# Performance work log

Measured on AMD Instinct MI355X. Metric: run time of the kernel, lower is better.

## Reference

```python
import jax, jax.numpy as jnp
import numpy as np

BN_EPS = 1e-5

def _conv(x, w, bias=None):
    # x: [N,C,H,W], w: [O,I,3,3], SAME padding, stride 1
    y = jax.lax.conv_general_dilated(x, w, window_strides=(1, 1),
                                     padding=((1, 1), (1, 1)),
                                     dimension_numbers=('NCHW', 'OIHW', 'NCHW'))
    if bias is not None:
        y = y + bias[None, :, None, None]
    return y

def _cconv(xr, xi, wr, wi):
    # complex conv: (xr + i xi) * (wr + i wi), cross-term combination
    return _conv(xr, wr) - _conv(xi, wi), _conv(xr, wi) + _conv(xi, wr)

def _bn1(x, g, b):
    # per-channel batchnorm (training-style stats over N,H,W)
    mu = jnp.mean(x, axis=(0, 2, 3), keepdims=True)
    var = jnp.var(x, axis=(0, 2, 3), keepdims=True)
    xh = (x - mu) * jax.lax.rsqrt(var + BN_EPS)
    return xh * g[None, :, None, None] + b[None, :, None, None]

def _cbn(xr, xi, g, b):
    # naive complex BN: normalize real/imag parts separately, shared affine
    return _bn1(xr, g, b), _bn1(xi, g, b)

def _crelu(xr, xi):
    return jax.nn.relu(xr), jax.nn.relu(xi)

def setup_inputs() -> dict:
    key = jax.random.key(0)
    ks = jax.random.split(key, 16)
    def w(k, o, i, kh=3, kw=3, s=0.05):
        return jax.random.normal(k, (o, i, kh, kw), jnp.float32) * s
    d = {}
    d['x'] = jax.random.normal(ks[0], (4, 256, 128, 224), jnp.float32)
    d['w1r'] = w(ks[1], 144, 256); d['w1i'] = w(ks[2], 144, 256)
    d['g1'] = jnp.ones((144,), jnp.float32); d['b1'] = jnp.zeros((144,), jnp.float32)
    d['w2r'] = w(ks[3], 96, 144); d['w2i'] = w(ks[4], 96, 144)
    d['g2'] = jnp.ones((96,), jnp.float32); d['b2'] = jnp.zeros((96,), jnp.float32)
    d['w3r'] = w(ks[5], 96, 96); d['w3i'] = w(ks[6], 96, 96)
    d['g3'] = jnp.ones((96,), jnp.float32); d['b3'] = jnp.zeros((96,), jnp.float32)
    d['w4r'] = w(ks[7], 96, 96); d['w4i'] = w(ks[8], 96, 96)
    d['g4'] = jnp.ones((96,), jnp.float32); d['b4'] = jnp.zeros((96,), jnp.float32)
    d['wc'] = w(ks[9], 1, 96); d['bc'] = jnp.zeros((1,), jnp.float32)
    d['wg'] = w(ks[10], 2, 96); d['bg'] = jnp.zeros((2,), jnp.float32)
    return d

def reference(x, w1r, w1i, g1, b1, w2r, w2i, g2, b2,
              w3r, w3i, g3, b3, w4r, w4i, g4, b4, wc, bc, wg, bg):
    # real input promoted to complex with zero imag
    xr, xi = x, jnp.zeros_like(x)
    xr, xi = _cconv(xr, xi, w1r, w1i)
    xr, xi = _cbn(xr, xi, g1, b1)
    xr, xi = _crelu(xr, xi)
    xr, xi = _cconv(xr, xi, w2r, w2i)
    xr, xi = _cbn(xr, xi, g2, b2)
    xr, xi = _crelu(xr, xi)
    xr, xi = _cconv(xr, xi, w3r, w3i)
    xr, xi = _cbn(xr, xi, g3, b3)
    xr, xi = _crelu(xr, xi)
    xr, xi = _cconv(xr, xi, w4r, w4i)
    xr, xi = _cbn(xr, xi, g4, b4)
    xr, xi = _crelu(xr, xi)
    x_mag = jnp.sqrt(xr * xr + xi * xi)  # torch.abs on complex
    cls = jax.nn.sigmoid(_conv(x_mag, wc, bc))
    reg = _conv(x_mag, wg, bg)
    return jnp.concatenate([cls, reg], axis=1)  # [N, 1+reg_layer, H, W]
```

## Files before the change

kernel.cpp:

```cpp
#include <hip/hip_runtime.h>
#include <cstdint>
#include <cstddef>

#define P_TOT 114688
#define W_IMG 224
#define H_IMG 128

typedef _Float16 f16;
typedef __attribute__((ext_vector_type(8))) _Float16 f16x8;
typedef __attribute__((ext_vector_type(4))) _Float16 f16x4;
typedef __attribute__((ext_vector_type(2))) _Float16 f16x2;
typedef __attribute__((ext_vector_type(4))) float f32x4;

#define WAITVM(N) asm volatile("s_waitcnt vmcnt(" #N ")" ::: "memory")

__device__ __forceinline__ void barrier_sync() {
  asm volatile("" ::: "memory");
  __builtin_amdgcn_s_barrier();
  asm volatile("" ::: "memory");
}

__device__ __forceinline__ void gload16(const void* g, void* l) {
  __builtin_amdgcn_global_load_lds((const __attribute__((address_space(1))) void*)g,
                                   (__attribute__((address_space(3))) void*)l, 16, 0, 0);
}

__global__ void k_pack_x(const float* __restrict__ x, f16* __restrict__ xb) {
  int tid = threadIdx.x;
  int pw  = tid & 15;
  int c8  = tid >> 4;
  int p   = blockIdx.x * 16 + pw;
  int w   = p % W_IMG;
  int h   = (p / W_IMG) % H_IMG;
  int n   = p / (H_IMG * W_IMG);
  const float* src = x + ((size_t)(n * 256 + c8 * 8) * H_IMG + h) * W_IMG + w;
  f16x8 v;
#pragma unroll
  for (int j = 0; j < 8; j++) v[j] = (f16)src[(size_t)j * (H_IMG * W_IMG)];
  int c8s = (c8 & ~3) | ((c8 ^ (w >> 1)) & 3);
  *(f16x8*)(xb + (size_t)p * 256 + c8s * 8) = v;
}

__global__ void k_pack_w(const float* __restrict__ wa, const float* __restrict__ wb,
                         f16* __restrict__ dst, int mode, int OT, int CS,
                         int Coh, int Cih, int total) {
  int gid = blockIdx.x * 256 + threadIdx.x;
  if (gid >= total) return;
  int j  = gid & 31;
  int t1 = gid >> 5;
  int o  = t1 % OT;
  int t2 = t1 / OT;
  int CCc = CS >> 5;
  int cc = t2 % CCc;
  int kk = t2 / CCc;
  int chunkT = ((j >> 3) ^ (o >> 1)) & 3;
  int is = cc * 32 + chunkT * 8 + (j & 7);
  float val = 0.f;
  if (mode == 0) {
    val = (o < Coh) ? wa[((size_t)o * Cih + is) * 9 + kk]
                    : wb[((size_t)(o - Coh) * Cih + is) * 9 + kk];
  } else if (mode == 1) {
    if (o < Coh) {
      val = (is < Cih) ? wa[((size_t)o * Cih + is) * 9 + kk]
                       : -wb[((size_t)o * Cih + (is - Cih)) * 9 + kk];
    } else {
      int oo = o - Coh;
      val = (is < Cih) ? wb[((size_t)oo * Cih + is) * 9 + kk]
                       : wa[((size_t)oo * Cih + (is - Cih)) * 9 + kk];
    }
  } else {
    if (o == 0)      val = wa[(size_t)is * 9 + kk];
    else if (o == 1) val = wb[(size_t)is * 9 + kk];
    else if (o == 2) val = wb[(size_t)(96 + is) * 9 + kk];
  }
  dst[gid] = (f16)val;
}

template<int BM, int OT, int CS, int WM, int WN, bool HEAD>
__launch_bounds__(WM * WN * 64)
__global__ void k_gemm(const f16* __restrict__ xb, const f16* __restrict__ Apack,
                       const char* __restrict__ zerop,
                       f16* __restrict__ y, float* __restrict__ outh,
                       const float* __restrict__ bcp, const float* __restrict__ bgp,
                       float* __restrict__ sums, float* __restrict__ sumsq) {
  constexpr int NT = WM * WN * 64;
  constexpr int NWV = NT / 64;
  constexpr int CC = CS / 32;
  constexpr int MF = BM / (WM * 16);
  constexpr int NF = 224 / (WN * 16);
  constexpr int NCH = 9 * CC;
  constexpr int TILE1 = (BM + 224) * 32;
  constexpr int ACH = BM * 64 / 1024;
  constexpr int TCH = ACH + 14;
  constexpr int NHALF = HEAD ? 1 : 2;
  static_assert(HEAD || (TCH % NWV == 0 && TCH / NWV == 5), "vmcnt math: 5 loads/thread/half");
  __shared__ f16 lds[2][NHALF * TILE1];

  constexpr int NOT = OT / BM;
  constexpr int nwg = NOT * 512;
  int bid = blockIdx.x;
  int swz = (bid & 7) * (nwg >> 3) + (bid >> 3);
  const int ot = swz % NOT;
  const int rq = swz / NOT;
  const int n = rq >> 7;
  const int h = rq & 127;
  const int tid  = threadIdx.x;
  const int lane = tid & 63;
  const int wv   = tid >> 6;
  const int wm   = wv % WM;
  const int wn   = wv / WM;
  const int obase  = wm * (MF * 16);
  const int wnbase = wn * (NF * 16);
  const int l15 = lane & 15;
  const int lhi = lane >> 4;
  const int aoff = l15 * 64 + (((lhi ^ (l15 >> 1)) & 3) << 4);

  f32x4 acc[MF][NF];
#pragma unroll
  for (int mi = 0; mi < MF; mi++)
#pragma unroll
    for (int ni = 0; ni < NF; ni++) acc[mi][ni] = (f32x4){0.f, 0.f, 0.f, 0.f};

  const size_t rowstride = (size_t)CS * 2;

  auto stage1 = [&](char* base, int q) {
    const int kk = q / CC, c = q % CC;
    const char* asrc = (const char*)(Apack + ((size_t)q * OT + ot * BM) * 32);
    const int dh = kk / 3 - 1;
    const int dw = kk % 3 - 1;
    const int hp = h + dh;
    const bool hok = (hp >= 0) && (hp < H_IMG);
    const int hpc = hok ? hp : 0;
    const char* brow = (const char*)xb + ((size_t)(n * H_IMG + hpc) * W_IMG) * rowstride + c * 64;
#pragma unroll
    for (int ck = wv; ck < TCH; ck += NWV) {
      char* dst = base + ck * 1024;
      if (ck < ACH) {
        gload16(asrc + ck * 1024 + lane * 16, dst);
      } else {
        int bidx = ck - ACH;
        int px = bidx * 16 + (lane >> 2);
        int ch = lane & 3;
        int wp = px + dw;
        bool ok = hok && ((unsigned)wp < 224u);
        const char* src = ok ? brow + (size_t)wp * rowstride + ch * 16
                             : zerop + ch * 16;
        gload16(src, dst);
      }
    }
  };

  auto compute_half = [&](const char* base, int kk) {
    const int dw = kk % 3 - 1;
    const char* Ab = base;
    const char* Bb = base + BM * 64;
    f16x8 af[MF], bfr[NF];
#pragma unroll
    for (int mi = 0; mi < MF; mi++)
      af[mi] = *(const f16x8*)(Ab + (obase + mi * 16) * 64 + aoff);
#pragma unroll
    for (int ni = 0; ni < NF; ni++) {
      int px = wnbase + ni * 16 + l15;
      int sw = ((lhi ^ ((px + dw) >> 1)) & 3) << 4;
      bfr[ni] = *(const f16x8*)(Bb + px * 64 + sw);
    }
    __builtin_amdgcn_s_setprio(1);
#pragma unroll
    for (int mi = 0; mi < MF; mi++)
#pragma unroll
      for (int ni = 0; ni < NF; ni++)
        acc[mi][ni] = __builtin_amdgcn_mfma_f32_16x16x32_f16(af[mi], bfr[ni], acc[mi][ni], 0, 0, 0);
    __builtin_amdgcn_s_setprio(0);
  };

  if constexpr (!HEAD) {
    constexpr int STEPS = (NCH + 1) / 2;
    auto stage_pair = [&](int buf, int q) {
      char* b = (char*)&lds[buf][0];
      int q1 = (q + 1 < NCH) ? (q + 1) : (NCH - 1);
      stage1(b, q);
      stage1(b + TILE1 * 2, q1);
    };
    stage_pair(0, 0);
    for (int s = 0; s < STEPS; ++s) {
      int qn = (s + 1) * 2;
      if (qn < NCH) { stage_pair((s + 1) & 1, qn); WAITVM(10); }
      else          { WAITVM(0); }
      barrier_sync();
      const char* b = (const char*)&lds[s & 1][0];
      int q = s * 2;
      compute_half(b, q / CC);
      if (q + 1 < NCH) compute_half(b + TILE1 * 2, (q + 1) / CC);
      barrier_sync();
    }
  } else {
    stage1((char*)&lds[0][0], 0);
    __syncthreads();
    int buf = 0;
    for (int t = 0; t < NCH; ++t) {
      int tn = t + 1;
      if (tn < NCH) stage1((char*)&lds[buf ^ 1][0], tn);
      compute_half((const char*)&lds[buf][0], t / CC);
      __syncthreads();
      buf ^= 1;
    }
  }

  const size_t prow = (size_t)(n * H_IMG + h) * W_IMG;
  if constexpr (!HEAD) {
#pragma unroll
    for (int mi = 0; mi < MF; mi++) {
#pragma unroll
      for (int ni = 0; ni < NF; ni++) {
        int o = obase + mi * 16 + lhi * 4;
        int w = wnbase + ni * 16 + l15;
        f16x4 v4;
#pragma unroll
        for (int j = 0; j < 4; j++) v4[j] = (f16)acc[mi][ni][j];
        *(f16x4*)(y + (prow + w) * OT + ot * BM + o) = v4;
      }
    }
    float sv[MF][4], qv[MF][4];
#pragma unroll
    for (int mi = 0; mi < MF; mi++)
#pragma unroll
      for (int j = 0; j < 4; j++) {
        float s = 0.f, q = 0.f;
#pragma unroll
        for (int ni = 0; ni < NF; ni++) {
          float v = acc[mi][ni][j];
          s += v; q += v * v;
        }
        sv[mi][j] = s; qv[mi][j] = q;
      }
#pragma unroll
    for (int m = 1; m < 16; m <<= 1) {
#pragma unroll
      for (int mi = 0; mi < MF; mi++)
#pragma unroll
        for (int j = 0; j < 4; j++) {
          sv[mi][j] += __shfl_xor(sv[mi][j], m);
          qv[mi][j] += __shfl_xor(qv[mi][j], m);
        }
    }
    if (l15 == 0) {
#pragma unroll
      for (int mi = 0; mi < MF; mi++)
#pragma unroll
        for (int j = 0; j < 4; j++) {
          int ch = ot * BM + obase + mi * 16 + lhi * 4 + j;
          atomicAdd(&sums[ch], sv[mi][j]);
          atomicAdd(&sumsq[ch], qv[mi][j]);
        }
    }
  } else {
    if (lhi == 0) {
      float b0 = bcp[0], b1 = bgp[0], b2 = bgp[1];
#pragma unroll
      for (int ni = 0; ni < NF; ni++) {
        int w = wnbase + ni * 16 + l15;
        float c0 = acc[0][ni][0] + b0;
        c0 = 1.f / (1.f + expf(-c0));
        float c1 = acc[0][ni][1] + b1;
        float c2 = acc[0][ni][2] + b2;
        outh[((size_t)(n * 3 + 0) * H_IMG + h) * W_IMG + w] = c0;
        outh[((size_t)(n * 3 + 1) * H_IMG + h) * W_IMG + w] = c1;
        outh[((size_t)(n * 3 + 2) * H_IMG + h) * W_IMG + w] = c2;
      }
    }
  }
}

template<int O>
__device__ __forceinline__ void bn_coef(const float* __restrict__ sums,
                                        const float* __restrict__ sumsq,
                                        const float* __restrict__ g,
                                        const float* __restrict__ b,
                                        float* sc, float* sh, int tid, int nt) {
  const float inv = 1.0f / (float)P_TOT;
  for (int t = tid; t < O; t += nt) {
    float mean = sums[t] * inv;
    float var  = fmaxf(sumsq[t] * inv - mean * mean, 0.f);
    int gi = (t < O / 2) ? t : (t - O / 2);
    float s = g[gi] * rsqrtf(var + 1e-5f);
    sc[t] = s;
    sh[t] = b[gi] - mean * s;
  }
}

template<int O>
__global__ void k_packip(f16* __restrict__ y,
                         const float* __restrict__ sums, const float* __restrict__ sumsq,
                         const float* __restrict__ g, const float* __restrict__ b) {
  __shared__ float sc[O], sh[O];
  bn_coef<O>(sums, sumsq, g, b, sc, sh, threadIdx.x, 256);
  __syncthreads();
  constexpr int G32 = O / 32;
  int gid = blockIdx.x * 256 + threadIdx.x;
  if (gid >= P_TOT * G32) return;
  int gg = gid % G32;
  int p = gid / G32;
  int w = p % W_IMG;
  f16* base = y + (size_t)p * O + gg * 32;
  f16x8 in[4];
#pragma unroll
  for (int ch = 0; ch < 4; ch++) in[ch] = *(const f16x8*)(base + ch * 8);
  int sw = (w >> 1) & 3;
  f16x8 outv[4];
#pragma unroll
  for (int ch = 0; ch < 4; ch++) {
#pragma unroll
    for (int j = 0; j < 8; j++) {
      int cdx = gg * 32 + ch * 8 + j;
      float f = fmaxf(fmaf((float)in[ch][j], sc[cdx], sh[cdx]), 0.f);
      outv[ch][j] = (f16)f;
    }
  }
#pragma unroll
  for (int ch = 0; ch < 4; ch++) *(f16x8*)(base + ((ch ^ sw) & 3) * 8) = outv[ch];
}

__global__ void k_mag(const f16* __restrict__ y,
                      const float* __restrict__ sums, const float* __restrict__ sumsq,
                      const float* __restrict__ g, const float* __restrict__ b,
                      f16* __restrict__ mg) {
  __shared__ float sc[192], sh[192];
  bn_coef<192>(sums, sumsq, g, b, sc, sh, threadIdx.x, 256);
  __syncthreads();
  int gid = blockIdx.x * 256 + threadIdx.x;
  if (gid >= P_TOT * 12) return;
  int c8 = gid % 12;
  int p  = gid / 12;
  int w  = p % W_IMG;
  f16x8 r8 = *(const f16x8*)(y + (size_t)p * 192 + c8 * 8);
  f16x8 i8 = *(const f16x8*)(y + (size_t)p * 192 + 96 + c8 * 8);
  f16x8 outv;
#pragma unroll
  for (int j = 0; j < 8; j++) {
    int cdx = c8 * 8 + j;
    float rr = fmaxf(fmaf((float)r8[j], sc[cdx], sh[cdx]), 0.f);
    float ii = fmaxf(fmaf((float)i8[j], sc[96 + cdx], sh[96 + cdx]), 0.f);
    outv[j] = (f16)sqrtf(rr * rr + ii * ii);
  }
  int c8s = (c8 & ~3) | ((c8 ^ (w >> 1)) & 3);
  *(f16x8*)(mg + (size_t)p * 96 + c8s * 8) = outv;
}

extern "C" void kernel_launch(void* const* d_in, const int* in_sizes, int n_in,
                              void* d_out, int out_size, void* d_ws, size_t ws_size,
                              hipStream_t stream) {
  const float* x   = (const float*)d_in[0];
  const float* w1r = (const float*)d_in[1];
  const float* w1i = (const float*)d_in[2];
  const float* g1  = (const float*)d_in[3];
  const float* b1  = (const float*)d_in[4];
  const float* w2r = (const float*)d_in[5];
  const float* w2i = (const float*)d_in[6];
  const float* g2  = (const float*)d_in[7];
  const float* b2  = (const float*)d_in[8];
  const float* w3r = (const float*)d_in[9];
  const float* w3i = (const float*)d_in[10];
  const float* g3  = (const float*)d_in[11];
  const float* b3  = (const float*)d_in[12];
  const float* w4r = (const float*)d_in[13];
  const float* w4i = (const float*)d_in[14];
  const float* g4  = (const float*)d_in[15];
  const float* b4  = (const float*)d_in[16];
  const float* wc  = (const float*)d_in[17];
  const float* bcp = (const float*)d_in[18];
  const float* wg  = (const float*)d_in[19];
  const float* bgp = (const float*)d_in[20];
  float* out = (float*)d_out;

  char* ws = (char*)d_ws;
  if (ws_size < 137500000ULL) return;

  char* zerop = ws;
  auto S  = [&](int L) { return (float*)(ws + 16384 + L * 4096); };
  auto Q  = [&](int L) { return (float*)(ws + 16384 + L * 4096) + 512; };
  f16* A1 = (f16*)(ws + 65536);
  f16* A2 = (f16*)(ws + 1392640);
  f16* A3 = (f16*)(ws + 2387968);
  f16* A4 = (f16*)(ws + 3051520);
  f16* AH = (f16*)(ws + 3715072);
  f16* XB0 = (f16*)(ws + (8ULL << 20));
  f16* Y   = (f16*)(ws + (68ULL << 20));

  hipMemsetAsync(d_ws, 0, 49152, stream);

  k_pack_x<<<P_TOT / 16, 512, 0, stream>>>(x, XB0);
  k_pack_w<<<(663552 + 255) / 256, 256, 0, stream>>>(w1r, w1i, A1, 0, 288, 256, 144, 256, 663552);
  k_pack_w<<<(497664 + 255) / 256, 256, 0, stream>>>(w2r, w2i, A2, 1, 192, 288, 96, 144, 497664);
  k_pack_w<<<(331776 + 255) / 256, 256, 0, stream>>>(w3r, w3i, A3, 1, 192, 192, 96, 96, 331776);
  k_pack_w<<<(331776 + 255) / 256, 256, 0, stream>>>(w4r, w4i, A4, 1, 192, 192, 96, 96, 331776);
  k_pack_w<<<(13824 + 255) / 256, 256, 0, stream>>>(wc, wg, AH, 2, 16, 96, 0, 96, 13824);

  k_gemm<96, 288, 256, 2, 2, false><<<1536, 256, 0, stream>>>(XB0, A1, zerop, Y, nullptr, nullptr, nullptr, S(0), Q(0));
  k_packip<288><<<P_TOT * 9 / 256, 256, 0, stream>>>(Y, S(0), Q(0), g1, b1);

  k_gemm<96, 192, 288, 2, 2, false><<<1024, 256, 0, stream>>>(Y, A2, zerop, XB0, nullptr, nullptr, nullptr, S(1), Q(1));
  k_packip<192><<<P_TOT * 6 / 256, 256, 0, stream>>>(XB0, S(1), Q(1), g2, b2);

  k_gemm<96, 192, 192, 2, 2, false><<<1024, 256, 0, stream>>>(XB0, A3, zerop, Y, nullptr, nullptr, nullptr, S(2), Q(2));
  k_packip<192><<<P_TOT * 6 / 256, 256, 0, stream>>>(Y, S(2), Q(2), g3, b3);

  k_gemm<96, 192, 192, 2, 2, false><<<1024, 256, 0, stream>>>(Y, A4, zerop, XB0, nullptr, nullptr, nullptr, S(3), Q(3));

  k_mag<<<P_TOT * 12 / 256, 256, 0, stream>>>(XB0, S(3), Q(3), g4, b4, Y);

  k_gemm<16, 16, 96, 1, 2, true><<<512, 128, 0, stream>>>(Y, AH, zerop, nullptr, out, bcp, bgp, nullptr, nullptr);

  (void)in_sizes; (void)n_in; (void)out_size;
}
```

Measured before the change: 901.4 us.

## Store activations in zero-padded halo slabs to drop boundary checks in loads

Activation buffers now use a padded layout (130x228 per image) whose halo ring is zeroed by a new small kernel before each layer. The GEMM's B-tile loader then reads from simple strided addresses with no per-lane bounds checks or redirects to a zero page. All producers and consumers index through the padded layout. This adds several small halo-clearing launches and slightly larger buffers in exchange for cheaper address generation in the inner staging loop.

```diff
diff --git a/kernel.cpp b/kernel.cpp
--- a/kernel.cpp
+++ b/kernel.cpp
@@ -5,11 +5,12 @@
 #define P_TOT 114688
 #define W_IMG 224
 #define H_IMG 128
+#define WP 228
+#define HP 130
 
 typedef _Float16 f16;
 typedef __attribute__((ext_vector_type(8))) _Float16 f16x8;
 typedef __attribute__((ext_vector_type(4))) _Float16 f16x4;
-typedef __attribute__((ext_vector_type(2))) _Float16 f16x2;
 typedef __attribute__((ext_vector_type(4))) float f32x4;
 
 #define WAITVM(N) asm volatile("s_waitcnt vmcnt(" #N ")" ::: "memory")
@@ -23,6 +24,24 @@
 __device__ __forceinline__ void gload16(const void* g, void* l) {
   __builtin_amdgcn_global_load_lds((const __attribute__((address_space(1))) void*)g,
                                    (__attribute__((address_space(3))) void*)l, 16, 0, 0);
+}
+
+__device__ __forceinline__ size_t pad_px(int n, int h, int w) {
+  return ((size_t)(n * HP + h + 1)) * WP + (w + 1);
+}
+
+__global__ void k_halo(f16* __restrict__ slab, int CS) {
+  int c8n = CS >> 3;
+  int tid = blockIdx.x * 256 + threadIdx.x;
+  int c8 = tid % c8n;
+  int rest = tid / c8n;
+  if (rest >= 4 * 968) return;
+  int n = rest / 968, i = rest % 968;
+  int h, w;
+  if (i < 456) { h = (i < 228) ? 0 : 129; w = i % 228; }
+  else { int j = i - 456; h = 1 + (j >> 2); int k = j & 3; w = (k == 0) ? 0 : (224 + k); }
+  size_t pp = ((size_t)(n * HP + h)) * WP + w;
+  *(f16x8*)(slab + pp * CS + c8 * 8) = (f16x8){0, 0, 0, 0, 0, 0, 0, 0};
 }
 
 __global__ void k_pack_x(const float* __restrict__ x, f16* __restrict__ xb) {
@@ -38,7 +57,7 @@
 #pragma unroll
   for (int j = 0; j < 8; j++) v[j] = (f16)src[(size_t)j * (H_IMG * W_IMG)];
   int c8s = (c8 & ~3) | ((c8 ^ (w >> 1)) & 3);
-  *(f16x8*)(xb + (size_t)p * 256 + c8s * 8) = v;
+  *(f16x8*)(xb + pad_px(n, h, w) * 256 + c8s * 8) = v;
 }
 
 __global__ void k_pack_w(const float* __restrict__ wa, const float* __restrict__ wb,
@@ -79,7 +98,6 @@
 template<int BM, int OT, int CS, int WM, int WN, bool HEAD>
 __launch_bounds__(WM * WN * 64)
 __global__ void k_gemm(const f16* __restrict__ xb, const f16* __restrict__ Apack,
-                       const char* __restrict__ zerop,
                        f16* __restrict__ y, float* __restrict__ outh,
                        const float* __restrict__ bcp, const float* __restrict__ bgp,
                        float* __restrict__ sums, float* __restrict__ sumsq) {
@@ -90,7 +108,7 @@
   constexpr int NF = 224 / (WN * 16);
   constexpr int NCH = 9 * CC;
   constexpr int TILE1 = (BM + 224) * 32;
-  constexpr int ACH = BM * 64 / 1024;
+  constexpr int ACH = BM / 16;
   constexpr int TCH = ACH + 14;
   constexpr int NHALF = HEAD ? 1 : 2;
   static_assert(HEAD || (TCH % NWV == 0 && TCH / NWV == 5), "vmcnt math: 5 loads/thread/half");
@@ -121,32 +139,21 @@
 #pragma unroll
     for (int ni = 0; ni < NF; ni++) acc[mi][ni] = (f32x4){0.f, 0.f, 0.f, 0.f};
 
-  const size_t rowstride = (size_t)CS * 2;
+  const char* abase = (const char*)Apack + (size_t)ot * BM * 64 + lane * 16;
+  const char* bbase = (const char*)xb +
+      (pad_px(n, h, 0) + (lane >> 2)) * (CS * 2) + (lane & 3) * 16;
 
   auto stage1 = [&](char* base, int q) {
     const int kk = q / CC, c = q % CC;
-    const char* asrc = (const char*)(Apack + ((size_t)q * OT + ot * BM) * 32);
     const int dh = kk / 3 - 1;
     const int dw = kk % 3 - 1;
-    const int hp = h + dh;
-    const bool hok = (hp >= 0) && (hp < H_IMG);
-    const int hpc = hok ? hp : 0;
-    const char* brow = (const char*)xb + ((size_t)(n * H_IMG + hpc) * W_IMG) * rowstride + c * 64;
+    const char* asrc = abase + (size_t)q * (OT * 64);
+    const char* bsrc = bbase + (dh * WP + dw) * (int)(CS * 2) + c * 64;
 #pragma unroll
     for (int ck = wv; ck < TCH; ck += NWV) {
       char* dst = base + ck * 1024;
-      if (ck < ACH) {
-        gload16(asrc + ck * 1024 + lane * 16, dst);
-      } else {
-        int bidx = ck - ACH;
-        int px = bidx * 16 + (lane >> 2);
-        int ch = lane & 3;
-        int wp = px + dw;
-        bool ok = hok && ((unsigned)wp < 224u);
-        const char* src = ok ? brow + (size_t)wp * rowstride + ch * 16
-                             : zerop + ch * 16;
-        gload16(src, dst);
-      }
+      if (ck < ACH) gload16(asrc + ck * 1024, dst);
+      else          gload16(bsrc + (size_t)(ck - ACH) * (16 * CS * 2), dst);
     }
   };
 
@@ -206,8 +213,8 @@
     }
   }
 
-  const size_t prow = (size_t)(n * H_IMG + h) * W_IMG;
   if constexpr (!HEAD) {
+    const size_t prow = pad_px(n, h, 0);
 #pragma unroll
     for (int mi = 0; mi < MF; mi++) {
 #pragma unroll
@@ -301,7 +308,9 @@
   int gg = gid % G32;
   int p = gid / G32;
   int w = p % W_IMG;
-  f16* base = y + (size_t)p * O + gg * 32;
+  int hh = (p / W_IMG) % H_IMG;
+  int nn = p / (W_IMG * H_IMG);
+  f16* base = y + pad_px(nn, hh, w) * O + gg * 32;
   f16x8 in[4];
 #pragma unroll
   for (int ch = 0; ch < 4; ch++) in[ch] = *(const f16x8*)(base + ch * 8);
@@ -332,8 +341,11 @@
   int c8 = gid % 12;
   int p  = gid / 12;
   int w  = p % W_IMG;
-  f16x8 r8 = *(const f16x8*)(y + (size_t)p * 192 + c8 * 8);
-  f16x8 i8 = *(const f16x8*)(y + (size_t)p * 192 + 96 + c8 * 8);
+  int hh = (p / W_IMG) % H_IMG;
+  int nn = p / (W_IMG * H_IMG);
+  size_t pp = pad_px(nn, hh, w);
+  f16x8 r8 = *(const f16x8*)(y + pp * 192 + c8 * 8);
+  f16x8 i8 = *(const f16x8*)(y + pp * 192 + 96 + c8 * 8);
   f16x8 outv;
 #pragma unroll
   for (int j = 0; j < 8; j++) {
@@ -343,7 +355,7 @@
     outv[j] = (f16)sqrtf(rr * rr + ii * ii);
   }
   int c8s = (c8 & ~3) | ((c8 ^ (w >> 1)) & 3);
-  *(f16x8*)(mg + (size_t)p * 96 + c8s * 8) = outv;
+  *(f16x8*)(mg + pp * 96 + c8s * 8) = outv;
 }
 
 extern "C" void kernel_launch(void* const* d_in, const int* in_sizes, int n_in,
@@ -375,7 +387,6 @@
   char* ws = (char*)d_ws;
   if (ws_size < 137500000ULL) return;
 
-  char* zerop = ws;
   auto S  = [&](int L) { return (float*)(ws + 16384 + L * 4096); };
   auto Q  = [&](int L) { return (float*)(ws + 16384 + L * 4096) + 512; };
   f16* A1 = (f16*)(ws + 65536);
@@ -383,32 +394,39 @@
   f16* A3 = (f16*)(ws + 2387968);
   f16* A4 = (f16*)(ws + 3051520);
   f16* AH = (f16*)(ws + 3715072);
-  f16* XB0 = (f16*)(ws + (8ULL << 20));
-  f16* Y   = (f16*)(ws + (68ULL << 20));
+  f16* SLA = (f16*)(ws + 4194304);
+  f16* SLB = (f16*)(ws + 65011712);
 
   hipMemsetAsync(d_ws, 0, 49152, stream);
 
-  k_pack_x<<<P_TOT / 16, 512, 0, stream>>>(x, XB0);
+  auto halo_grid = [](int CS) { return (4 * 968 * (CS / 8) + 255) / 256; };
+
+  k_halo<<<halo_grid(256), 256, 0, stream>>>(SLA, 256);
+  k_pack_x<<<P_TOT / 16, 512, 0, stream>>>(x, SLA);
   k_pack_w<<<(663552 + 255) / 256, 256, 0, stream>>>(w1r, w1i, A1, 0, 288, 256, 144, 256, 663552);
   k_pack_w<<<(497664 + 255) / 256, 256, 0, stream>>>(w2r, w2i, A2, 1, 192, 288, 96, 144, 497664);
   k_pack_w<<<(331776 + 255) / 256, 256, 0, stream>>>(w3r, w3i, A3, 1, 192, 192, 96, 96, 331776);
   k_pack_w<<<(331776 + 255) / 256, 256, 0, stream>>>(w4r, w4i, A4, 1, 192, 192, 96, 96, 331776);
   k_pack_w<<<(13824 + 255) / 256, 256, 0, stream>>>(wc, wg, AH, 2, 16, 96, 0, 96, 13824);
-
-  k_gemm<96, 288, 256, 2, 2, false><<<1536, 256, 0, stream>>>(XB0, A1, zerop, Y, nullptr, nullptr, nullptr, S(0), Q(0));
-  k_packip<288><<<P_TOT * 9 / 256, 256, 0, stream>>>(Y, S(0), Q(0), g1, b1);
-
-  k_gemm<96, 192, 288, 2, 2, false><<<1024, 256, 0, stream>>>(Y, A2, zerop, XB0, nullptr, nullptr, nullptr, S(1), Q(1));
-  k_packip<192><<<P_TOT * 6 / 256, 256, 0, stream>>>(XB0, S(1), Q(1), g2, b2);
-
-  k_gemm<96, 192, 192, 2, 2, false><<<1024, 256, 0, stream>>>(XB0, A3, zerop, Y, nullptr, nullptr, nullptr, S(2), Q(2));
-  k_packip<192><<<P_TOT * 6 / 256, 256, 0, stream>>>(Y, S(2), Q(2), g3, b3);
-
-  k_gemm<96, 192, 192, 2, 2, false><<<1024, 256, 0, stream>>>(Y, A4, zerop, XB0, nullptr, nullptr, nullptr, S(3), Q(3));
-
-  k_mag<<<P_TOT * 12 / 256, 256, 0, stream>>>(XB0, S(3), Q(3), g4, b4, Y);
-
-  k_gemm<16, 16, 96, 1, 2, true><<<512, 128, 0, stream>>>(Y, AH, zerop, nullptr, out, bcp, bgp, nullptr, nullptr);
+  k_halo<<<halo_grid(288), 256, 0, stream>>>(SLB, 288);
+
+  k_gemm<96, 288, 256, 2, 2, false><<<1536, 256, 0, stream>>>(SLA, A1, SLB, nullptr, nullptr, nullptr, S(0), Q(0));
+  k_packip<288><<<P_TOT * 9 / 256, 256, 0, stream>>>(SLB, S(0), Q(0), g1, b1);
+  k_halo<<<halo_grid(192), 256, 0, stream>>>(SLA, 192);
+
+  k_gemm<96, 192, 288, 2, 2, false><<<1024, 256, 0, stream>>>(SLB, A2, SLA, nullptr, nullptr, nullptr, S(1), Q(1));
+  k_packip<192><<<P_TOT * 6 / 256, 256, 0, stream>>>(SLA, S(1), Q(1), g2, b2);
+  k_halo<<<halo_grid(192), 256, 0, stream>>>(SLB, 192);
+
+  k_gemm<96, 192, 192, 2, 2, false><<<1024, 256, 0, stream>>>(SLA, A3, SLB, nullptr, nullptr, nullptr, S(2), Q(2));
+  k_packip<192><<<P_TOT * 6 / 256, 256, 0, stream>>>(SLB, S(2), Q(2), g3, b3);
+
+  k_gemm<96, 192, 192, 2, 2, false><<<1024, 256, 0, stream>>>(SLB, A4, SLA, nullptr, nullptr, nullptr, S(3), Q(3));
+  k_halo<<<halo_grid(96), 256, 0, stream>>>(SLB, 96);
+
+  k_mag<<<P_TOT * 12 / 256, 256, 0, stream>>>(SLA, S(3), Q(3), g4, b4, SLB);
+
+  k_gemm<16, 16, 96, 1, 2, true><<<512, 128, 0, stream>>>(SLB, AH, nullptr, out, bcp, bgp, nullptr, nullptr);
 
   (void)in_sizes; (void)n_in; (void)out_size;
 }
```

Result: no change. 883.7 us (-2.0%).
